# Performance work log

Measured on AMD Instinct MI355X. Metric: run time of the kernel, lower is better.

## Reference

```python
import jax, jax.numpy as jnp
import numpy as np

B, N, D = 8, 2048, 128

def setup_inputs() -> dict:
    key = jax.random.key(0)
    k1, k2, k3 = jax.random.split(key, 3)
    embeddings = jax.random.normal(k1, (B, N, D), dtype=jnp.float32)
    cost_matrix = jax.random.uniform(k2, (B, N, N), dtype=jnp.float32)
    W = jax.random.normal(k3, (D, 2 * D), dtype=jnp.float32) * (1.0 / np.sqrt(2 * D))
    b = jnp.zeros((D,), dtype=jnp.float32)
    return {"embeddings": embeddings, "cost_matrix": cost_matrix, "W": W, "b": b}

def reference(embeddings, cost_matrix, W, b):
    # degree[b,j] = number of nonzero entries in row j of cost_matrix
    degree = (cost_matrix != 0).astype(embeddings.dtype).sum(axis=-1)  # [B,N]
    # sum_neighbors[b,j,d] = sum_i embeddings[b,i,d] * cost_matrix[b,i,j]
    # (algebraic rewrite of the O(B*N*N*D) broadcast-multiply-reduce)
    sum_neighbors = jnp.einsum('bij,bid->bjd', cost_matrix, embeddings)
    sum_neighbors = sum_neighbors / degree[..., None]
    concatenated = jnp.concatenate([embeddings, sum_neighbors], axis=-1)  # [B,N,2D]
    return jax.nn.relu(jnp.einsum('bnf,df->bnd', concatenated, W) + b)
```

## Files before the change

kernel.cpp:

```cpp
#include <hip/hip_runtime.h>
#include <stdint.h>

#define B_ 8
#define N_ 2048
#define D_ 128
#define NT_ 32
#define KT_ 16
#define TILE_BYTES 16384
#define PS_ ((size_t)B_ * N_ * D_)

typedef unsigned short u16;
typedef unsigned int u32;
using f32x4 = __attribute__((ext_vector_type(4))) float;
using bf16x8 = __attribute__((ext_vector_type(8))) short;
using u16x8 = __attribute__((ext_vector_type(8))) u16;

__device__ inline u16 f2bf(float x) {
  u32 u = __float_as_uint(x);
  return (u16)((u + 0x7FFFu + ((u >> 16) & 1u)) >> 16);
}
__device__ inline float bf2f(u16 h) { return __uint_as_float((u32)h << 16); }

__device__ inline void glds16(const void* g, void* l) {
  __builtin_amdgcn_global_load_lds((const __attribute__((address_space(1))) void*)g,
                                   (__attribute__((address_space(3))) void*)l, 16, 0, 0);
}

__global__ __launch_bounds__(256) void prep_et_kernel(const float* __restrict__ E,
                                                      u16* __restrict__ ETsw) {
  __shared__ float Els[64][132];
  const int blk = blockIdx.x;
  const int b = blk >> 5;
  const int g = blk & 31;
  const int t = threadIdx.x;
  const float* Eb = E + ((size_t)b * N_ + g * 64) * D_;
#pragma unroll
  for (int s = 0; s < 8; ++s) {
    const int f4 = t + 256 * s;
    const int r = f4 >> 5;
    const int c4 = f4 & 31;
    f32x4 v = *(const f32x4*)(Eb + (size_t)r * D_ + c4 * 4);
#pragma unroll
    for (int e = 0; e < 4; ++e) Els[r][c4 * 4 + e] = v[e];
  }
  __syncthreads();
  u16* img = ETsw + ((size_t)b * NT_ + g) * (TILE_BYTES / 2);
  const int d = t >> 1;
  const int swz = (d ^ (d >> 3)) & 7;
#pragma unroll
  for (int gg = 0; gg < 4; ++gg) {
    const int grp = (t & 1) * 4 + gg;
    u16x8 pk;
#pragma unroll
    for (int e = 0; e < 8; ++e) pk[e] = f2bf(Els[grp * 8 + e][d]);
    *(u16x8*)(img + d * 64 + ((grp ^ swz) << 3)) = pk;
  }
}

__global__ __launch_bounds__(256) void prep_w_kernel(const float* __restrict__ W,
                                                     u16* __restrict__ Wsw) {
  const int t = threadIdx.x;
  const int d = t >> 1;
  const int swz = (d ^ (d >> 3)) & 7;
#pragma unroll
  for (int s = 0; s < 16; ++s) {
    const int k8 = (t & 1) * 16 + s;
    f32x4 v0 = *(const f32x4*)(W + d * 256 + k8 * 8);
    f32x4 v1 = *(const f32x4*)(W + d * 256 + k8 * 8 + 4);
    u16x8 pk;
#pragma unroll
    for (int e = 0; e < 4; ++e) { pk[e] = f2bf(v0[e]); pk[4 + e] = f2bf(v1[e]); }
    *(u16x8*)(Wsw + d * 256 + ((k8 ^ swz) << 3)) = pk;
  }
}

__global__ __launch_bounds__(256) void gemm_kernel(const float* __restrict__ C,
                                                   const u16* __restrict__ ETsw,
                                                   u16* __restrict__ Sp,
                                                   int* __restrict__ deg) {
  __shared__ __align__(16) u16 Asw[2][64 * 64];
  __shared__ __align__(16) u16 Bsw[2][128 * 64];
  const int phys = blockIdx.x;
  const int orig = (phys & 7) * 64 + (phys >> 3);
  const int b = orig >> 6;
  const int ks = (orig >> 5) & 1;
  const int jt = orig & 31;
  const int j0 = jt * 64;
  const int t = threadIdx.x;
  const int lane = t & 63;
  const int wave = t >> 6;
  const int wm = wave >> 1, wn = wave & 1;
  const int lm = lane & 15, lh = lane >> 4;
  const int aRow = t >> 4, aCol = t & 15;

  const float* Cb = C + (size_t)b * N_ * N_;
  const char* Eimg = (const char*)(ETsw + (size_t)b * NT_ * (TILE_BYTES / 2));
  int* degb = deg + b * N_;
  const int g0 = ks * KT_;

  f32x4 acc[2][4];
#pragma unroll
  for (int i = 0; i < 2; ++i)
#pragma unroll
    for (int j = 0; j < 4; ++j) acc[i][j] = (f32x4)0.0f;
  f32x4 av[4];

#define ISSUE_B(gi, buf)                                                          \
  {                                                                               \
    _Pragma("unroll") for (int s = 0; s < 4; ++s) {                               \
      const int chunk = s * 4 + wave;                                             \
      glds16(Eimg + (size_t)(gi)*TILE_BYTES + chunk * 1024 + lane * 16,           \
             (char*)&Bsw[buf][0] + chunk * 1024);                                 \
    }                                                                             \
  }
#define LOAD_A(gi)                                                                \
  {                                                                               \
    _Pragma("unroll") for (int s = 0; s < 4; ++s) av[s] =                         \
        *(const f32x4*)(Cb + (size_t)((gi)*64 + aRow + 16 * s) * N_ + j0 + aCol * 4); \
  }
#define WRITE_A(gi, buf)                                                          \
  {                                                                               \
    _Pragma("unroll") for (int s = 0; s < 4; ++s) {                               \
      const int i = aRow + 16 * s;                                                \
      f32x4 v = av[s];                                                            \
      int cnt = (v[0] != 0.0f) + (v[1] != 0.0f) + (v[2] != 0.0f) + (v[3] != 0.0f);\
      cnt += __shfl_xor(cnt, 1);                                                  \
      cnt += __shfl_xor(cnt, 2);                                                  \
      cnt += __shfl_xor(cnt, 4);                                                  \
      cnt += __shfl_xor(cnt, 8);                                                  \
      if ((lane & 15) == 0) atomicAdd(&degb[(gi)*64 + i], cnt);                   \
      _Pragma("unroll") for (int e = 0; e < 4; ++e) {                             \
        const int jl = aCol * 4 + e;                                              \
        const int sz = (jl ^ (jl >> 3)) & 7;                                      \
        Asw[buf][jl * 64 + (i ^ (sz << 3))] = f2bf(v[e]);                         \
      }                                                                           \
    }                                                                             \
  }
#define MFMA_PHASE(buf)                                                           \
  {                                                                               \
    bf16x8 af[2][2], bfr[4][2];                                                   \
    _Pragma("unroll") for (int fm = 0; fm < 2; ++fm) {                            \
      const int jl = wm * 32 + fm * 16 + lm;                                      \
      const int sz = (jl ^ (jl >> 3)) & 7;                                        \
      _Pragma("unroll") for (int kf = 0; kf < 2; ++kf) {                          \
        const int K8 = kf * 32 + lh * 8;                                          \
        af[fm][kf] = *(const bf16x8*)&Asw[buf][jl * 64 + (K8 ^ (sz << 3))];       \
      }                                                                           \
    }                                                                             \
    _Pragma("unroll") for (int fn = 0; fn < 4; ++fn) {                            \
      const int nl = wn * 64 + fn * 16 + lm;                                      \
      const int sz = (nl ^ (nl >> 3)) & 7;                                        \
      _Pragma("unroll") for (int kf = 0; kf < 2; ++kf) {                          \
        const int K8 = kf * 32 + lh * 8;                                          \
        bfr[fn][kf] = *(const bf16x8*)&Bsw[buf][nl * 64 + (K8 ^ (sz << 3))];      \
      }                                                                           \
    }                                                                             \
    _Pragma("unroll") for (int kf = 0; kf < 2; ++kf)                              \
        _Pragma("unroll") for (int fm = 0; fm < 2; ++fm)                          \
        _Pragma("unroll") for (int fn = 0; fn < 4; ++fn) acc[fm][fn] =            \
        __builtin_amdgcn_mfma_f32_16x16x32_bf16(af[fm][kf], bfr[fn][kf],          \
                                                acc[fm][fn], 0, 0, 0);            \
  }

  ISSUE_B(g0, 0);
  LOAD_A(g0);
  WRITE_A(g0, 0);
  LOAD_A(g0 + 1);
  asm volatile("s_waitcnt lgkmcnt(0)" ::: "memory");
  __builtin_amdgcn_sched_barrier(0);
  __builtin_amdgcn_s_barrier();
  __builtin_amdgcn_sched_barrier(0);

  int cur = 0;
  for (int kt = 0; kt < KT_ - 1; ++kt) {
    ISSUE_B(g0 + kt + 1, cur ^ 1);
    __builtin_amdgcn_sched_barrier(0);
    MFMA_PHASE(cur);
    __builtin_amdgcn_sched_barrier(0);
    WRITE_A(g0 + kt + 1, cur ^ 1);
    __builtin_amdgcn_sched_barrier(0);
    if (kt < KT_ - 2) LOAD_A(g0 + kt + 2);
    __builtin_amdgcn_sched_barrier(0);
    asm volatile("s_waitcnt vmcnt(8)" ::: "memory");
    asm volatile("s_waitcnt lgkmcnt(0)" ::: "memory");
    __builtin_amdgcn_sched_barrier(0);
    __builtin_amdgcn_s_barrier();
    __builtin_amdgcn_sched_barrier(0);
    cur ^= 1;
  }
  MFMA_PHASE(cur);

  u16* Sb = Sp + (size_t)ks * PS_ + ((size_t)b * N_ + j0) * D_;
#pragma unroll
  for (int fm = 0; fm < 2; ++fm)
#pragma unroll
    for (int fn = 0; fn < 4; ++fn)
#pragma unroll
      for (int r = 0; r < 4; ++r) {
        const int row = wm * 32 + fm * 16 + lh * 4 + r;
        const int col = wn * 64 + fn * 16 + lm;
        Sb[(size_t)row * D_ + col] = f2bf(acc[fm][fn][r]);
      }
#undef ISSUE_B
#undef LOAD_A
#undef WRITE_A
#undef MFMA_PHASE
}

__global__ __launch_bounds__(256) void out_kernel(const float* __restrict__ E,
                                                  const u16* __restrict__ Sp,
                                                  const int* __restrict__ deg,
                                                  const u16* __restrict__ Wsw,
                                                  const float* __restrict__ bias,
                                                  float* __restrict__ out) {
  __shared__ __align__(16) u16 Wls[128 * 256];
  __shared__ __align__(16) u16 Als[32 * 256];
  const int r0 = blockIdx.x * 32;
  const int t = threadIdx.x;
  const int lane = t & 63;
  const int wave = t >> 6;
  const int lm = lane & 15, lh = lane >> 4;

#pragma unroll
  for (int s = 0; s < 16; ++s) {
    const int chunk = s * 4 + wave;
    glds16((const char*)Wsw + chunk * 1024 + lane * 16, (char*)Wls + chunk * 1024);
  }
  const int r = t >> 3, gq = t & 7;
  const int swzr = (r ^ (r >> 3)) & 7;
  const float idg = 1.0f / (float)deg[r0 + r];
  const float* Er = E + (size_t)(r0 + r) * D_;
#pragma unroll
  for (int h = 0; h < 2; ++h) {
    const int k8 = gq + 8 * h;
    f32x4 v0 = *(const f32x4*)(Er + k8 * 8);
    f32x4 v1 = *(const f32x4*)(Er + k8 * 8 + 4);
    u16x8 pk;
#pragma unroll
    for (int e = 0; e < 4; ++e) { pk[e] = f2bf(v0[e]); pk[4 + e] = f2bf(v1[e]); }
    *(u16x8*)&Als[r * 256 + ((k8 ^ swzr) << 3)] = pk;
  }
  const size_t off = (size_t)(r0 + r) * D_;
#pragma unroll
  for (int h = 0; h < 2; ++h) {
    const int kq = gq + 8 * h;
    u16x8 p0 = *(const u16x8*)(Sp + off + kq * 8);
    u16x8 p1 = *(const u16x8*)(Sp + PS_ + off + kq * 8);
    u16x8 pk;
#pragma unroll
    for (int e = 0; e < 8; ++e) pk[e] = f2bf((bf2f(p0[e]) + bf2f(p1[e])) * idg);
    *(u16x8*)&Als[r * 256 + (((16 + kq) ^ swzr) << 3)] = pk;
  }
  __syncthreads();

  f32x4 acc[2][2];
#pragma unroll
  for (int i = 0; i < 2; ++i)
#pragma unroll
    for (int j = 0; j < 2; ++j) acc[i][j] = (f32x4)0.0f;
  const int dbase = wave * 32;
#pragma unroll
  for (int kf = 0; kf < 8; ++kf) {
    bf16x8 af[2], bfr[2];
#pragma unroll
    for (int fm = 0; fm < 2; ++fm) {
      const int rr = fm * 16 + lm;
      const int sz = (rr ^ (rr >> 3)) & 7;
      af[fm] = *(const bf16x8*)&Als[rr * 256 + (((kf * 4 + lh) ^ sz) << 3)];
    }
#pragma unroll
    for (int fn = 0; fn < 2; ++fn) {
      const int d = dbase + fn * 16 + lm;
      const int sz = (d ^ (d >> 3)) & 7;
      bfr[fn] = *(const bf16x8*)&Wls[d * 256 + (((kf * 4 + lh) ^ sz) << 3)];
    }
#pragma unroll
    for (int fm = 0; fm < 2; ++fm)
#pragma unroll
      for (int fn = 0; fn < 2; ++fn)
        acc[fm][fn] = __builtin_amdgcn_mfma_f32_16x16x32_bf16(af[fm], bfr[fn],
                                                              acc[fm][fn], 0, 0, 0);
  }
  float bb[2] = {bias[dbase + lm], bias[dbase + 16 + lm]};
#pragma unroll
  for (int fm = 0; fm < 2; ++fm)
#pragma unroll
    for (int fn = 0; fn < 2; ++fn)
#pragma unroll
      for (int rr = 0; rr < 4; ++rr) {
        const int row = r0 + fm * 16 + lh * 4 + rr;
        const int d = dbase + fn * 16 + lm;
        float x = acc[fm][fn][rr] + bb[fn];
        out[(size_t)row * D_ + d] = x > 0.0f ? x : 0.0f;
      }
}

extern "C" void kernel_launch(void* const* d_in, const int* in_sizes, int n_in,
                              void* d_out, int out_size, void* d_ws, size_t ws_size,
                              hipStream_t stream) {
  (void)in_sizes; (void)n_in; (void)out_size; (void)ws_size;
  const float* E = (const float*)d_in[0];
  const float* C = (const float*)d_in[1];
  const float* W = (const float*)d_in[2];
  const float* bias = (const float*)d_in[3];
  float* out = (float*)d_out;

  char* ws = (char*)d_ws;
  int* deg = (int*)ws;
  u16* ETsw = (u16*)(ws + 65536);
  u16* Wsw = (u16*)(ws + 65536 + 4194304);
  u16* Sp = (u16*)(ws + 65536 + 4194304 + 65536);

  hipMemsetAsync(deg, 0, B_ * N_ * sizeof(int), stream);
  hipLaunchKernelGGL(prep_et_kernel, dim3(256), dim3(256), 0, stream, E, ETsw);
  hipLaunchKernelGGL(prep_w_kernel, dim3(1), dim3(256), 0, stream, W, Wsw);
  hipLaunchKernelGGL(gemm_kernel, dim3(512), dim3(256), 0, stream, C, ETsw, Sp, deg);
  hipLaunchKernelGGL(out_kernel, dim3(512), dim3(256), 0, stream, E, Sp, deg, Wsw, bias, out);
}
```

Baseline: 229.0 us.

## Count zeros instead of nonzeros to skip degree atomics, merge prep kernels

Degree is now derived as N minus a zero count, so the per-row shuffle reduction and atomics run only when a wave sees a zero entry. The W conversion is folded into the embedding prep kernel as an extra block, removing one launch. The GEMM main loop peels its final iteration so the wait count can be tightened to vmcnt(4) without a conditional load. Inputs with many zeros would incur scattered per-lane atomics instead of one per row segment.

```diff
diff --git a/kernel.cpp b/kernel.cpp
--- a/kernel.cpp
+++ b/kernel.cpp
@@ -26,13 +26,30 @@
                                    (__attribute__((address_space(3))) void*)l, 16, 0, 0);
 }
 
-__global__ __launch_bounds__(256) void prep_et_kernel(const float* __restrict__ E,
-                                                      u16* __restrict__ ETsw) {
+__global__ __launch_bounds__(256) void prep_kernel(const float* __restrict__ E,
+                                                   const float* __restrict__ W,
+                                                   u16* __restrict__ ETsw,
+                                                   u16* __restrict__ Wsw) {
+  const int blk = blockIdx.x;
+  const int t = threadIdx.x;
+  if (blk == 256) {
+    const int d = t >> 1;
+    const int swz = (d ^ (d >> 3)) & 7;
+#pragma unroll
+    for (int s = 0; s < 16; ++s) {
+      const int k8 = (t & 1) * 16 + s;
+      f32x4 v0 = *(const f32x4*)(W + d * 256 + k8 * 8);
+      f32x4 v1 = *(const f32x4*)(W + d * 256 + k8 * 8 + 4);
+      u16x8 pk;
+#pragma unroll
+      for (int e = 0; e < 4; ++e) { pk[e] = f2bf(v0[e]); pk[4 + e] = f2bf(v1[e]); }
+      *(u16x8*)(Wsw + d * 256 + ((k8 ^ swz) << 3)) = pk;
+    }
+    return;
+  }
   __shared__ float Els[64][132];
-  const int blk = blockIdx.x;
   const int b = blk >> 5;
   const int g = blk & 31;
-  const int t = threadIdx.x;
   const float* Eb = E + ((size_t)b * N_ + g * 64) * D_;
 #pragma unroll
   for (int s = 0; s < 8; ++s) {
@@ -57,27 +74,10 @@
   }
 }
 
-__global__ __launch_bounds__(256) void prep_w_kernel(const float* __restrict__ W,
-                                                     u16* __restrict__ Wsw) {
-  const int t = threadIdx.x;
-  const int d = t >> 1;
-  const int swz = (d ^ (d >> 3)) & 7;
-#pragma unroll
-  for (int s = 0; s < 16; ++s) {
-    const int k8 = (t & 1) * 16 + s;
-    f32x4 v0 = *(const f32x4*)(W + d * 256 + k8 * 8);
-    f32x4 v1 = *(const f32x4*)(W + d * 256 + k8 * 8 + 4);
-    u16x8 pk;
-#pragma unroll
-    for (int e = 0; e < 4; ++e) { pk[e] = f2bf(v0[e]); pk[4 + e] = f2bf(v1[e]); }
-    *(u16x8*)(Wsw + d * 256 + ((k8 ^ swz) << 3)) = pk;
-  }
-}
-
 __global__ __launch_bounds__(256) void gemm_kernel(const float* __restrict__ C,
                                                    const u16* __restrict__ ETsw,
                                                    u16* __restrict__ Sp,
-                                                   int* __restrict__ deg) {
+                                                   int* __restrict__ zeros) {
   __shared__ __align__(16) u16 Asw[2][64 * 64];
   __shared__ __align__(16) u16 Bsw[2][128 * 64];
   const int phys = blockIdx.x;
@@ -95,7 +95,7 @@
 
   const float* Cb = C + (size_t)b * N_ * N_;
   const char* Eimg = (const char*)(ETsw + (size_t)b * NT_ * (TILE_BYTES / 2));
-  int* degb = deg + b * N_;
+  int* zb = zeros + b * N_;
   const int g0 = ks * KT_;
 
   f32x4 acc[2][4];
@@ -123,12 +123,10 @@
     _Pragma("unroll") for (int s = 0; s < 4; ++s) {                               \
       const int i = aRow + 16 * s;                                                \
       f32x4 v = av[s];                                                            \
-      int cnt = (v[0] != 0.0f) + (v[1] != 0.0f) + (v[2] != 0.0f) + (v[3] != 0.0f);\
-      cnt += __shfl_xor(cnt, 1);                                                  \
-      cnt += __shfl_xor(cnt, 2);                                                  \
-      cnt += __shfl_xor(cnt, 4);                                                  \
-      cnt += __shfl_xor(cnt, 8);                                                  \
-      if ((lane & 15) == 0) atomicAdd(&degb[(gi)*64 + i], cnt);                   \
+      int zc = (v[0] == 0.0f) + (v[1] == 0.0f) + (v[2] == 0.0f) + (v[3] == 0.0f);\
+      if (__any(zc)) {                         \
+        if (zc) atomicAdd(&zb[(gi)*64 + i], zc);                                  \
+      }                                                                           \
       _Pragma("unroll") for (int e = 0; e < 4; ++e) {                             \
         const int jl = aCol * 4 + e;                                              \
         const int sz = (jl ^ (jl >> 3)) & 7;                                      \
@@ -172,22 +170,34 @@
   __builtin_amdgcn_sched_barrier(0);
 
   int cur = 0;
-  for (int kt = 0; kt < KT_ - 1; ++kt) {
+  for (int kt = 0; kt < KT_ - 2; ++kt) {
     ISSUE_B(g0 + kt + 1, cur ^ 1);
     __builtin_amdgcn_sched_barrier(0);
     MFMA_PHASE(cur);
     __builtin_amdgcn_sched_barrier(0);
     WRITE_A(g0 + kt + 1, cur ^ 1);
     __builtin_amdgcn_sched_barrier(0);
-    if (kt < KT_ - 2) LOAD_A(g0 + kt + 2);
-    __builtin_amdgcn_sched_barrier(0);
-    asm volatile("s_waitcnt vmcnt(8)" ::: "memory");
+    LOAD_A(g0 + kt + 2);
+    __builtin_amdgcn_sched_barrier(0);
+    asm volatile("s_waitcnt vmcnt(4)" ::: "memory");
     asm volatile("s_waitcnt lgkmcnt(0)" ::: "memory");
     __builtin_amdgcn_sched_barrier(0);
     __builtin_amdgcn_s_barrier();
     __builtin_amdgcn_sched_barrier(0);
     cur ^= 1;
   }
+  ISSUE_B(g0 + KT_ - 1, cur ^ 1);
+  __builtin_amdgcn_sched_barrier(0);
+  MFMA_PHASE(cur);
+  __builtin_amdgcn_sched_barrier(0);
+  WRITE_A(g0 + KT_ - 1, cur ^ 1);
+  __builtin_amdgcn_sched_barrier(0);
+  asm volatile("s_waitcnt vmcnt(0)" ::: "memory");
+  asm volatile("s_waitcnt lgkmcnt(0)" ::: "memory");
+  __builtin_amdgcn_sched_barrier(0);
+  __builtin_amdgcn_s_barrier();
+  __builtin_amdgcn_sched_barrier(0);
+  cur ^= 1;
   MFMA_PHASE(cur);
 
   u16* Sb = Sp + (size_t)ks * PS_ + ((size_t)b * N_ + j0) * D_;
@@ -209,7 +219,7 @@
 
 __global__ __launch_bounds__(256) void out_kernel(const float* __restrict__ E,
                                                   const u16* __restrict__ Sp,
-                                                  const int* __restrict__ deg,
+                                                  const int* __restrict__ zeros,
                                                   const u16* __restrict__ Wsw,
                                                   const float* __restrict__ bias,
                                                   float* __restrict__ out) {
@@ -228,7 +238,7 @@
   }
   const int r = t >> 3, gq = t & 7;
   const int swzr = (r ^ (r >> 3)) & 7;
-  const float idg = 1.0f / (float)deg[r0 + r];
+  const float idg = 1.0f / (2048.0f - (float)zeros[r0 + r]);
   const float* Er = E + (size_t)(r0 + r) * D_;
 #pragma unroll
   for (int h = 0; h < 2; ++h) {
@@ -306,14 +316,13 @@
   float* out = (float*)d_out;
 
   char* ws = (char*)d_ws;
-  int* deg = (int*)ws;
+  int* zeros = (int*)ws;
   u16* ETsw = (u16*)(ws + 65536);
   u16* Wsw = (u16*)(ws + 65536 + 4194304);
   u16* Sp = (u16*)(ws + 65536 + 4194304 + 65536);
 
-  hipMemsetAsync(deg, 0, B_ * N_ * sizeof(int), stream);
-  hipLaunchKernelGGL(prep_et_kernel, dim3(256), dim3(256), 0, stream, E, ETsw);
-  hipLaunchKernelGGL(prep_w_kernel, dim3(1), dim3(256), 0, stream, W, Wsw);
-  hipLaunchKernelGGL(gemm_kernel, dim3(512), dim3(256), 0, stream, C, ETsw, Sp, deg);
-  hipLaunchKernelGGL(out_kernel, dim3(512), dim3(256), 0, stream, E, Sp, deg, Wsw, bias, out);
-}
+  hipMemsetAsync(zeros, 0, B_ * N_ * sizeof(int), stream);
+  hipLaunchKernelGGL(prep_kernel, dim3(257), dim3(256), 0, stream, E, W, ETsw, Wsw);
+  hipLaunchKernelGGL(gemm_kernel, dim3(512), dim3(256), 0, stream, C, ETsw, Sp, zeros);
+  hipLaunchKernelGGL(out_kernel, dim3(512), dim3(256), 0, stream, E, Sp, zeros, Wsw, bias, out);
+}
```

Result: faster. 221.8 us (-3.1%).
